# Kernel optimization log

Measured on AMD Instinct MI355X. Metric: run time of the kernel, lower is better.

Reference implementation:

```python
import jax, jax.numpy as jnp
import numpy as np

B, IN, H, K = 4096, 1024, 1024, 32  # batch, input_size, hidden_size, inner_hidden


def setup_inputs() -> dict:
    key = jax.random.key(0)
    ks = jax.random.split(key, 11)
    stdv = 1.0 / np.sqrt(H)
    u = lambda k, shp: jax.random.uniform(k, shp, jnp.float32, -stdv, stdv)
    return {
        "x": jax.random.normal(ks[0], (B, IN), jnp.float32),
        "h_prev": jax.random.normal(ks[1], (B, H), jnp.float32),
        "c_prev": jax.random.normal(ks[2], (B, H), jnp.float32),
        "Wg": u(ks[3], (3 * H, IN + H)),
        "bg": u(ks[4], (3 * H,)),
        "Wc": u(ks[5], (2 * H, IN + H)),
        "bc": u(ks[6], (2 * H,)),
        "W1": u(ks[7], (K, 2)),
        "b1": u(ks[8], (K,)),
        "W2": u(ks[9], (1, K)),
        "b2": u(ks[10], (1,)),
    }


def reference(x, h_prev, c_prev, Wg, bg, Wc, bc, W1, b1, W2, b2):
    combined = jnp.concatenate([x, h_prev], axis=1)          # [B, IN+H]
    gates = combined @ Wg.T + bg                              # [B, 3H]
    i, f, o = jnp.split(jax.nn.sigmoid(gates), 3, axis=1)     # each [B, H]
    cell_raw = combined @ Wc.T + bc                           # [B, 2H]
    pairs = cell_raw.reshape(B, H, 2)                         # [B, H, 2]
    hid = jax.nn.relu(jnp.einsum('bhp,kp->bhk', pairs, W1) + b1)  # [B, H, K]
    g = jnp.einsum('bhk,ok->bho', hid, W2)[..., 0] + b2[0]    # [B, H]
    c_next = f * c_prev + i * g
    h_next = o * jnp.tanh(c_next)
    return (h_next, c_next)
```

## Files before the change

### kernel.cpp

```cpp
#include <hip/hip_runtime.h>
#include <hip/hip_bf16.h>

#define BB   4096
#define INW  1024
#define HH   1024
#define KIN  2048
#define NG   5120
#define KH   32

typedef __bf16 bf16;
typedef __bf16 bf16x4 __attribute__((ext_vector_type(4)));
typedef __bf16 bf16x8 __attribute__((ext_vector_type(8)));
typedef float  floatx4 __attribute__((ext_vector_type(4)));

#define GLD16(gp, lp)                                                          \
  __builtin_amdgcn_global_load_lds(                                            \
      (__attribute__((address_space(1))) const void*)(gp),                     \
      (__attribute__((address_space(3))) void*)(lp), 16, 0, 0)

#define NC4  (BB * KIN / 4)
#define NW8  (NG * KIN / 8)

__global__ __launch_bounds__(256) void prep(
    const float* __restrict__ x, const float* __restrict__ h,
    const float* __restrict__ Wg, const float* __restrict__ Wc,
    bf16* __restrict__ comb, bf16* __restrict__ Wb) {
  int i = blockIdx.x * 256 + threadIdx.x;
  if (i < NC4) {
    int e = i * 4;
    int b = e >> 11;
    int c = e & (KIN - 1);
    const float* src = (c < INW) ? (x + (size_t)b * INW + c)
                                 : (h + (size_t)b * HH + (c - INW));
    float4 v = *(const float4*)src;
    bf16x4 o4;
    o4[0] = (bf16)v.x; o4[1] = (bf16)v.y; o4[2] = (bf16)v.z; o4[3] = (bf16)v.w;
    *(bf16x4*)(comb + e) = o4;
  } else {
    int o = i - NC4;
    if (o < NW8) {
      int lane = o & 63;
      int f    = (o >> 6) & 7;
      int kk   = (o >> 9) & 63;
      int nt   = o >> 15;
      int n = nt * 128 + f * 16 + (lane & 15);
      int k = kk * 32 + (lane >> 4) * 8;
      const float* src = (n < 3 * HH) ? (Wg + (size_t)n * KIN + k)
                                      : (Wc + (size_t)(n - 3 * HH) * KIN + k);
      float4 v0 = *(const float4*)src;
      float4 v1 = *(const float4*)(src + 4);
      bf16x8 ov;
      ov[0] = (bf16)v0.x; ov[1] = (bf16)v0.y; ov[2] = (bf16)v0.z; ov[3] = (bf16)v0.w;
      ov[4] = (bf16)v1.x; ov[5] = (bf16)v1.y; ov[6] = (bf16)v1.z; ov[7] = (bf16)v1.w;
      *(bf16x8*)(Wb + (size_t)o * 8) = ov;
    }
  }
}

__global__ __launch_bounds__(256, 3) void gemm_bt(
    const bf16* __restrict__ A, const bf16* __restrict__ Bm,
    bf16* __restrict__ C) {
  __shared__ bf16 As[128 * 64];

  const int tid  = threadIdx.x;
  const int wave = tid >> 6;
  const int lane = tid & 63;
  const int m0 = blockIdx.x * 128;
  const int nt = blockIdx.y;

  const int wm = (wave >> 1) * 64;
  const int wn = (wave & 1) * 64;
  const int lr = lane & 15;
  const int qd = lane >> 4;
  const int sw = lr & 7;

  const bf16* Bq = Bm + (size_t)nt * (64 * 8 * 64 * 8)
                      + (size_t)((wave & 1) * 4) * 512 + (size_t)lane * 8;

  floatx4 acc[4][4] = {};

  for (int kt = 0; kt < KIN / 64; ++kt) {
    const int k0 = kt * 64;

    bf16x8 bfr[2][4];
#pragma unroll
    for (int ks = 0; ks < 2; ++ks)
#pragma unroll
      for (int ni = 0; ni < 4; ++ni)
        bfr[ks][ni] = *(const bf16x8*)(Bq + (((kt * 2 + ks) * 8 + ni) << 9));

    __syncthreads();
#pragma unroll
    for (int j = 0; j < 4; ++j) {
      int q   = j * 256 + tid;
      int row = q >> 3;
      int c   = (q & 7) ^ (row & 7);
      GLD16(A + (size_t)(m0 + row) * KIN + k0 + c * 8,
            As + (size_t)(j * 256 + wave * 64) * 8);
    }
    __syncthreads();

#pragma unroll
    for (int ks = 0; ks < 2; ++ks) {
      bf16x8 af[4];
#pragma unroll
      for (int mi = 0; mi < 4; ++mi)
        af[mi] = *(const bf16x8*)
            &As[(((wm + mi * 16 + lr) << 3) + ((ks * 4 + qd) ^ sw)) << 3];
#pragma unroll
      for (int mi = 0; mi < 4; ++mi)
#pragma unroll
        for (int ni = 0; ni < 4; ++ni)
          acc[mi][ni] = __builtin_amdgcn_mfma_f32_16x16x32_bf16(
              af[mi], bfr[ks][ni], acc[mi][ni], 0, 0, 0);
    }
  }

#pragma unroll
  for (int mi = 0; mi < 4; ++mi)
#pragma unroll
    for (int ni = 0; ni < 4; ++ni) {
      size_t base = (size_t)(m0 + wm + mi * 16 + qd * 4) * NG
                    + ((size_t)nt * 128 + wn + ni * 16 + lr);
#pragma unroll
      for (int r = 0; r < 4; ++r)
        C[base + (size_t)r * NG] = (bf16)acc[mi][ni][r];
    }
}

__global__ __launch_bounds__(256) void epilogue(
    const bf16* __restrict__ G, const float* __restrict__ c_prev,
    const float* __restrict__ bg, const float* __restrict__ bc,
    const float* __restrict__ W1, const float* __restrict__ b1,
    const float* __restrict__ W2, const float* __restrict__ b2,
    float* __restrict__ h_next, float* __restrict__ c_next) {
  int idx = blockIdx.x * 256 + threadIdx.x;
  int b = idx >> 10;
  int h = idx & (HH - 1);
  const bf16* Gr = G + (size_t)b * NG;

  float gi = (float)Gr[h]          + bg[h];
  float gf = (float)Gr[HH + h]     + bg[HH + h];
  float go = (float)Gr[2 * HH + h] + bg[2 * HH + h];
  float p0 = (float)Gr[3 * HH + 2 * h]     + bc[2 * h];
  float p1 = (float)Gr[3 * HH + 2 * h + 1] + bc[2 * h + 1];

  float g = b2[0];
#pragma unroll
  for (int k = 0; k < KH; ++k) {
    float hv = fmaf(p0, W1[2 * k], fmaf(p1, W1[2 * k + 1], b1[k]));
    hv = fmaxf(hv, 0.0f);
    g = fmaf(hv, W2[k], g);
  }

  float si = 1.0f / (1.0f + __expf(-gi));
  float sf = 1.0f / (1.0f + __expf(-gf));
  float so = 1.0f / (1.0f + __expf(-go));

  float cn = sf * c_prev[idx] + si * g;
  float hn = so * tanhf(cn);
  h_next[idx] = hn;
  c_next[idx] = cn;
}

extern "C" void kernel_launch(void* const* d_in, const int* in_sizes, int n_in,
                              void* d_out, int out_size, void* d_ws, size_t ws_size,
                              hipStream_t stream) {
  const float* x      = (const float*)d_in[0];
  const float* h_prev = (const float*)d_in[1];
  const float* c_prev = (const float*)d_in[2];
  const float* Wg     = (const float*)d_in[3];
  const float* bg     = (const float*)d_in[4];
  const float* Wc     = (const float*)d_in[5];
  const float* bc     = (const float*)d_in[6];
  const float* W1     = (const float*)d_in[7];
  const float* b1     = (const float*)d_in[8];
  const float* W2     = (const float*)d_in[9];
  const float* b2     = (const float*)d_in[10];
  float* out = (float*)d_out;

  char* ws = (char*)d_ws;
  bf16* comb = (bf16*)ws;
  bf16* Wb   = (bf16*)(ws + (size_t)BB * KIN * 2);
  bf16* G    = (bf16*)(ws + (size_t)BB * KIN * 2
                          + (size_t)NG * KIN * 2);

  prep<<<(NC4 + NW8 + 255) / 256, 256, 0, stream>>>(x, h_prev, Wg, Wc, comb, Wb);

  dim3 grid(BB / 128, NG / 128);
  gemm_bt<<<grid, 256, 0, stream>>>(comb, Wb, G);

  epilogue<<<(BB * HH) / 256, 256, 0, stream>>>(
      G, c_prev, bg, bc, W1, b1, W2, b2, out, out + (size_t)BB * HH);
}
```

Baseline: 254.3 us.

## Pre-swizzle activations into MFMA fragment layout and drop LDS staging in GEMM

The prep kernel now writes the bf16 activation matrix in per-fragment tile order, the same way the weights were already packed. The GEMM then loads both A and B fragments directly from global memory with coalesced 16-byte loads, using a two-stage register double buffer. This removes the LDS staging and both barriers per k-step. The cost is that the A tile is no longer shared through LDS: each wave re-reads its fragments from global or L2, which doubles the A traffic across the two N-waves, and more registers are in use.

```diff
diff --git a/kernel.cpp b/kernel.cpp
--- a/kernel.cpp
+++ b/kernel.cpp
@@ -13,31 +13,30 @@
 typedef __bf16 bf16x8 __attribute__((ext_vector_type(8)));
 typedef float  floatx4 __attribute__((ext_vector_type(4)));
 
-#define GLD16(gp, lp)                                                          \
-  __builtin_amdgcn_global_load_lds(                                            \
-      (__attribute__((address_space(1))) const void*)(gp),                     \
-      (__attribute__((address_space(3))) void*)(lp), 16, 0, 0)
-
-#define NC4  (BB * KIN / 4)
+#define NA8  (BB * KIN / 8)
 #define NW8  (NG * KIN / 8)
 
 __global__ __launch_bounds__(256) void prep(
     const float* __restrict__ x, const float* __restrict__ h,
     const float* __restrict__ Wg, const float* __restrict__ Wc,
-    bf16* __restrict__ comb, bf16* __restrict__ Wb) {
+    bf16* __restrict__ Ab, bf16* __restrict__ Wb) {
   int i = blockIdx.x * 256 + threadIdx.x;
-  if (i < NC4) {
-    int e = i * 4;
-    int b = e >> 11;
-    int c = e & (KIN - 1);
-    const float* src = (c < INW) ? (x + (size_t)b * INW + c)
-                                 : (h + (size_t)b * HH + (c - INW));
-    float4 v = *(const float4*)src;
-    bf16x4 o4;
-    o4[0] = (bf16)v.x; o4[1] = (bf16)v.y; o4[2] = (bf16)v.z; o4[3] = (bf16)v.w;
-    *(bf16x4*)(comb + e) = o4;
+  if (i < NA8) {
+    int lane = i & 63;
+    int kk   = (i >> 6) & 63;
+    int mt   = i >> 12;
+    int m = mt * 16 + (lane & 15);
+    int k = kk * 32 + (lane >> 4) * 8;
+    const float* src = (k < INW) ? (x + (size_t)m * INW + k)
+                                 : (h + (size_t)m * HH + (k - INW));
+    float4 v0 = *(const float4*)src;
+    float4 v1 = *(const float4*)(src + 4);
+    bf16x8 ov;
+    ov[0] = (bf16)v0.x; ov[1] = (bf16)v0.y; ov[2] = (bf16)v0.z; ov[3] = (bf16)v0.w;
+    ov[4] = (bf16)v1.x; ov[5] = (bf16)v1.y; ov[6] = (bf16)v1.z; ov[7] = (bf16)v1.w;
+    *(bf16x8*)(Ab + (size_t)i * 8) = ov;
   } else {
-    int o = i - NC4;
+    int o = i - NA8;
     if (o < NW8) {
       int lane = o & 63;
       int f    = (o >> 6) & 7;
@@ -57,11 +56,9 @@
   }
 }
 
-__global__ __launch_bounds__(256, 3) void gemm_bt(
+__global__ __launch_bounds__(256, 3) void gemm_ff(
     const bf16* __restrict__ A, const bf16* __restrict__ Bm,
     bf16* __restrict__ C) {
-  __shared__ bf16 As[128 * 64];
-
   const int tid  = threadIdx.x;
   const int wave = tid >> 6;
   const int lane = tid & 63;
@@ -72,48 +69,44 @@
   const int wn = (wave & 1) * 64;
   const int lr = lane & 15;
   const int qd = lane >> 4;
-  const int sw = lr & 7;
 
-  const bf16* Bq = Bm + (size_t)nt * (64 * 8 * 64 * 8)
-                      + (size_t)((wave & 1) * 4) * 512 + (size_t)lane * 8;
+  const bf16* Ap = A + (size_t)((m0 + wm) >> 4) * 32768 + lane * 8;
+  const bf16* Bp = Bm + (size_t)nt * 262144 + (size_t)(wave & 1) * 2048 + lane * 8;
 
   floatx4 acc[4][4] = {};
+  bf16x8 a0[4], b0[4], a1[4], b1[4];
 
-  for (int kt = 0; kt < KIN / 64; ++kt) {
-    const int k0 = kt * 64;
+#pragma unroll
+  for (int i = 0; i < 4; ++i) {
+    a0[i] = *(const bf16x8*)(Ap + i * 32768);
+    b0[i] = *(const bf16x8*)(Bp + i * 512);
+  }
 
-    bf16x8 bfr[2][4];
+  for (int kk = 0; kk < 64; kk += 2) {
 #pragma unroll
-    for (int ks = 0; ks < 2; ++ks)
+    for (int i = 0; i < 4; ++i) {
+      a1[i] = *(const bf16x8*)(Ap + i * 32768 + (kk + 1) * 512);
+      b1[i] = *(const bf16x8*)(Bp + (size_t)(kk + 1) * 4096 + i * 512);
+    }
+#pragma unroll
+    for (int mi = 0; mi < 4; ++mi)
 #pragma unroll
       for (int ni = 0; ni < 4; ++ni)
-        bfr[ks][ni] = *(const bf16x8*)(Bq + (((kt * 2 + ks) * 8 + ni) << 9));
-
-    __syncthreads();
+        acc[mi][ni] = __builtin_amdgcn_mfma_f32_16x16x32_bf16(
+            a0[mi], b0[ni], acc[mi][ni], 0, 0, 0);
+    if (kk + 2 < 64) {
 #pragma unroll
-    for (int j = 0; j < 4; ++j) {
-      int q   = j * 256 + tid;
-      int row = q >> 3;
-      int c   = (q & 7) ^ (row & 7);
-      GLD16(A + (size_t)(m0 + row) * KIN + k0 + c * 8,
-            As + (size_t)(j * 256 + wave * 64) * 8);
+      for (int i = 0; i < 4; ++i) {
+        a0[i] = *(const bf16x8*)(Ap + i * 32768 + (kk + 2) * 512);
+        b0[i] = *(const bf16x8*)(Bp + (size_t)(kk + 2) * 4096 + i * 512);
+      }
     }
-    __syncthreads();
-
 #pragma unroll
-    for (int ks = 0; ks < 2; ++ks) {
-      bf16x8 af[4];
+    for (int mi = 0; mi < 4; ++mi)
 #pragma unroll
-      for (int mi = 0; mi < 4; ++mi)
-        af[mi] = *(const bf16x8*)
-            &As[(((wm + mi * 16 + lr) << 3) + ((ks * 4 + qd) ^ sw)) << 3];
-#pragma unroll
-      for (int mi = 0; mi < 4; ++mi)
-#pragma unroll
-        for (int ni = 0; ni < 4; ++ni)
-          acc[mi][ni] = __builtin_amdgcn_mfma_f32_16x16x32_bf16(
-              af[mi], bfr[ks][ni], acc[mi][ni], 0, 0, 0);
-    }
+      for (int ni = 0; ni < 4; ++ni)
+        acc[mi][ni] = __builtin_amdgcn_mfma_f32_16x16x32_bf16(
+            a1[mi], b1[ni], acc[mi][ni], 0, 0, 0);
   }
 
 #pragma unroll
@@ -180,15 +173,15 @@
   float* out = (float*)d_out;
 
   char* ws = (char*)d_ws;
-  bf16* comb = (bf16*)ws;
-  bf16* Wb   = (bf16*)(ws + (size_t)BB * KIN * 2);
-  bf16* G    = (bf16*)(ws + (size_t)BB * KIN * 2
-                          + (size_t)NG * KIN * 2);
+  bf16* Ab = (bf16*)ws;
+  bf16* Wb = (bf16*)(ws + (size_t)BB * KIN * 2);
+  bf16* G  = (bf16*)(ws + (size_t)BB * KIN * 2
+                        + (size_t)NG * KIN * 2);
 
-  prep<<<(NC4 + NW8 + 255) / 256, 256, 0, stream>>>(x, h_prev, Wg, Wc, comb, Wb);
+  prep<<<(NA8 + NW8 + 255) / 256, 256, 0, stream>>>(x, h_prev, Wg, Wc, Ab, Wb);
 
   dim3 grid(BB / 128, NG / 128);
-  gemm_bt<<<grid, 256, 0, stream>>>(comb, Wb, G);
+  gemm_ff<<<grid, 256, 0, stream>>>(Ab, Wb, G);
 
   epilogue<<<(BB * HH) / 256, 256, 0, stream>>>(
       G, c_prev, bg, bc, W1, b1, W2, b2, out, out + (size_t)BB * HH);
```

Result: slower. 278.7 us (+9.6%).
